# Kernel tuning notes

Hardware: AMD Instinct MI355X
Metric: run time of the kernel (lower is better)

The kernel has to match this reference:

```python
import jax, jax.numpy as jnp
import numpy as np

N = 100000   # nodes
E = 3200000  # edges (avg degree 32)
D = 128      # embed_dim
H = 512      # FF hidden
EPS = 1e-5   # BatchNorm eps


def setup_inputs() -> dict:
    key = jax.random.key(0)
    ks = jax.random.split(key, 10)
    x = jax.random.normal(ks[0], (N, D), dtype=jnp.float32)
    edge_index = jax.random.randint(ks[1], (2, E), 0, N, dtype=jnp.int32)
    s = 1.0 / np.sqrt(D)
    W = jax.random.uniform(ks[2], (D, D), jnp.float32, -s, s)   # GCNConv weight
    b = jnp.zeros((D,), jnp.float32)                             # GCNConv bias
    gamma = jnp.ones((D,), jnp.float32)                          # shared BN affine
    beta = jnp.zeros((D,), jnp.float32)
    s1 = 1.0 / np.sqrt(D)
    w1 = jax.random.uniform(ks[3], (D, H), jnp.float32, -s1, s1)
    b1 = jax.random.uniform(ks[4], (H,), jnp.float32, -s1, s1)
    s2 = 1.0 / np.sqrt(H)
    w2 = jax.random.uniform(ks[5], (H, D), jnp.float32, -s2, s2)
    b2 = jax.random.uniform(ks[6], (D,), jnp.float32, -s2, s2)
    return {"x": x, "edge_index": edge_index, "W": W, "b": b,
            "gamma": gamma, "beta": beta, "w1": w1, "b1": b1, "w2": w2, "b2": b2}


def batchnorm(x, gamma, beta):
    # training-mode BatchNorm1d over node dim, biased variance
    mu = jnp.mean(x, axis=0)
    var = jnp.mean(jnp.square(x - mu), axis=0)
    return (x - mu) * jax.lax.rsqrt(var + EPS) * gamma + beta


def gcn_conv(x, edge_index, W, b):
    # PyG GCNConv: add self-loops, sym-normalize, linear, scatter-add, bias
    n = x.shape[0]
    loops = jnp.arange(n, dtype=edge_index.dtype)
    src = jnp.concatenate([edge_index[0], loops])
    dst = jnp.concatenate([edge_index[1], loops])
    xw = x @ W                                                    # [N, D]
    deg = jax.ops.segment_sum(jnp.ones_like(dst, x.dtype), dst, num_segments=n)
    dinv = jax.lax.rsqrt(deg)                                     # deg >= 1 (self-loops)
    norm = dinv[src] * dinv[dst]                                  # [E+N]
    msg = xw[src] * norm[:, None]                                 # [E+N, D] gather
    out = jax.ops.segment_sum(msg, dst, num_segments=n)           # scatter-add
    return out + b


def reference(x, edge_index, W, b, gamma, beta, w1, b1, w2, b2):
    h = gcn_conv(x, edge_index, W, b)
    x = batchnorm(x + h, gamma, beta)
    ff = jax.nn.relu(x @ w1 + b1) @ w2 + b2
    return batchnorm(x + ff, gamma, beta)
```

## Files before the change

kernel.cpp:

```cpp
#include <hip/hip_runtime.h>
#include <hip/hip_bf16.h>
#include <stdint.h>

#define NN 100000
#define NE 3200000
#define DIM 128
#define HID 512
#define BN_EPS 1e-5f
#define NBIN 16
#define NPBIN 6250
#define TILE 2048
#define CAP 210000
#define GCNT 16

typedef short short8 __attribute__((ext_vector_type(8)));
typedef float floatx4 __attribute__((ext_vector_type(4)));

__device__ __forceinline__ float bfu2f(unsigned short u) {
    return __uint_as_float(((unsigned int)u) << 16);
}
__device__ __forceinline__ unsigned short f2bfu(float f) {
    union { __hip_bfloat16 h; unsigned short u; } cv;
    cv.h = __float2bfloat16(f);
    return cv.u;
}

__global__ void k_init(int* __restrict__ bincur, float* __restrict__ stats) {
    int i = blockIdx.x * 256 + threadIdx.x;
    if (i < NBIN) bincur[i] = i * CAP;
    if (i < 512) stats[i] = 0.f;
}

__global__ __launch_bounds__(256) void k_fill1(const int* __restrict__ src, const int* __restrict__ dst,
                                               int* __restrict__ bincur, unsigned int* __restrict__ recs) {
    __shared__ int lhist[NBIN], lbase[NBIN], gbase[NBIN];
    __shared__ unsigned int lrec[TILE];
    int tid = threadIdx.x;
    int tbase = blockIdx.x * TILE;
    if (tid < NBIN) lhist[tid] = 0;
    __syncthreads();
    unsigned int myrec[8];
    int mybin[8], myrank[8];
    #pragma unroll
    for (int j = 0; j < 8; ++j) {
        int e = tbase + j * 256 + tid;
        mybin[j] = -1;
        if (e < NE) {
            int d = __builtin_nontemporal_load(dst + e);
            int s = __builtin_nontemporal_load(src + e);
            int b = d / NPBIN;
            myrec[j] = (unsigned)s | ((unsigned)(d - b * NPBIN) << 17);
            mybin[j] = b;
            myrank[j] = atomicAdd(&lhist[b], 1);
        }
    }
    __syncthreads();
    if (tid == 0) {
        int run = 0;
        #pragma unroll
        for (int b = 0; b < NBIN; ++b) { lbase[b] = run; run += lhist[b]; }
    }
    __syncthreads();
    if (tid < NBIN) gbase[tid] = atomicAdd(&bincur[tid], lhist[tid]);
    __syncthreads();
    #pragma unroll
    for (int j = 0; j < 8; ++j)
        if (mybin[j] >= 0) lrec[lbase[mybin[j]] + myrank[j]] = myrec[j];
    __syncthreads();
    int total = lbase[NBIN - 1] + lhist[NBIN - 1];
    for (int i = tid; i < total; i += 256) {
        int b = 0;
        #pragma unroll
        for (int st = 8; st > 0; st >>= 1)
            if (b + st < NBIN && lbase[b + st] <= i) b += st;
        int p = gbase[b] + (i - lbase[b]);
        if (p < (b + 1) * CAP) recs[p] = lrec[i];
    }
}

__global__ __launch_bounds__(256) void k_cnt(const unsigned int* __restrict__ recs,
                                             const int* __restrict__ bincur,
                                             int* __restrict__ part) {
    __shared__ int lhist[NPBIN];
    int b = blockIdx.x & (NBIN - 1);
    int g = blockIdx.x >> 4;
    int tid = threadIdx.x;
    for (int i = tid; i < NPBIN; i += 256) lhist[i] = 0;
    __syncthreads();
    int start = b * CAP;
    int end = bincur[b];
    if (end > start + CAP) end = start + CAP;
    if (end < start) end = start;
    int n = end - start;
    int per = (n + GCNT - 1) / GCNT;
    int cbeg = start + g * per;
    int cend = min(cbeg + per, end);
    for (int i = cbeg + tid; i < cend; i += 256) {
        unsigned int r = __builtin_nontemporal_load(recs + i);
        int dl = (int)(r >> 17);
        if (dl < NPBIN) atomicAdd(&lhist[dl], 1);
    }
    __syncthreads();
    int* pp = part + (size_t)(b * GCNT + g) * NPBIN;
    for (int i = tid; i < NPBIN; i += 256) pp[i] = lhist[i];
}

__global__ void k_sum(const int* __restrict__ part, int* __restrict__ cnt) {
    int n = blockIdx.x * 256 + threadIdx.x;
    if (n < NN) {
        int b = n / NPBIN, dl = n - b * NPBIN;
        const int* pp = part + (size_t)b * GCNT * NPBIN + dl;
        int s = 0;
        #pragma unroll
        for (int g = 0; g < GCNT; ++g) s += pp[g * NPBIN];
        cnt[n] = s;
    }
}

__global__ __launch_bounds__(1024) void k_scanA(const int* __restrict__ cnt, int* __restrict__ offs,
                                                int* __restrict__ bsum, float* __restrict__ dinv) {
    __shared__ int wsum[16];
    int t = threadIdx.x;
    int lane = t & 63, wid = t >> 6;
    int i = blockIdx.x * 1024 + t;
    int v = (i < NN) ? cnt[i] : 0;
    int incl = v;
    #pragma unroll
    for (int off = 1; off < 64; off <<= 1) {
        int y = __shfl_up(incl, off, 64);
        if (lane >= off) incl += y;
    }
    if (lane == 63) wsum[wid] = incl;
    __syncthreads();
    if (wid == 0) {
        int wv = (lane < 16) ? wsum[lane] : 0;
        int wincl = wv;
        #pragma unroll
        for (int off = 1; off < 16; off <<= 1) {
            int y = __shfl_up(wincl, off, 64);
            if (lane >= off) wincl += y;
        }
        if (lane < 16) wsum[lane] = wincl - wv;
    }
    __syncthreads();
    int excl = wsum[wid] + incl - v;
    if (i < NN) {
        offs[i] = excl;
        dinv[i] = rsqrtf((float)(v + 1));
    }
    if (t == 1023) bsum[blockIdx.x] = excl + v;
}

__global__ __launch_bounds__(128) void k_scanB(int* __restrict__ bsum, int* __restrict__ offs, int nblk) {
    int t = threadIdx.x;
    if (t < 64) {
        int v = (t < nblk) ? bsum[t] : 0;
        int v2 = (t + 64 < nblk) ? bsum[t + 64] : 0;
        int incl = v;
        #pragma unroll
        for (int off = 1; off < 64; off <<= 1) {
            int y = __shfl_up(incl, off, 64);
            if (t >= off) incl += y;
        }
        int tot0 = __shfl(incl, 63, 64);
        int incl2 = v2;
        #pragma unroll
        for (int off = 1; off < 64; off <<= 1) {
            int y = __shfl_up(incl2, off, 64);
            if (t >= off) incl2 += y;
        }
        if (t < nblk) bsum[t] = incl - v;
        if (t + 64 < nblk) bsum[t + 64] = tot0 + incl2 - v2;
        if (t == 63) offs[NN] = tot0 + __shfl(incl2, 63, 64);
    }
}

__global__ void k_scanC(int* __restrict__ offs, const int* __restrict__ bsum, int* __restrict__ cur) {
    int i = blockIdx.x * 256 + threadIdx.x;
    if (i < NN) {
        int o = offs[i] + bsum[i >> 10];
        offs[i] = o;
        cur[i] = o;
    }
}

__global__ __launch_bounds__(256) void k_fill2(const unsigned int* __restrict__ recs,
                                               const int* __restrict__ bincur,
                                               int* __restrict__ cur, int* __restrict__ srcs) {
    int b = (blockIdx.x & 7) | (((blockIdx.x >> 3) & 1) << 3);
    int g = blockIdx.x >> 4;
    int lo = b * NPBIN;
    int start = b * CAP;
    int end = bincur[b];
    if (end > start + CAP) end = start + CAP;
    if (end < start) end = start;
    int nrec = end - start;
    int per = (nrec + 31) / 32;
    int cbeg = start + g * per;
    int cend = min(cbeg + per, end);
    for (int i = cbeg + threadIdx.x; i < cend; i += 256) {
        unsigned int r = __builtin_nontemporal_load(recs + i);
        int s = (int)(r & 0x1FFFFu);
        int d = lo + (int)(r >> 17);
        int p = atomicAdd(&cur[d], 1);
        if ((unsigned)p < NE) srcs[p] = s;
    }
}

__global__ void k_wt(const float* __restrict__ W, unsigned short* __restrict__ wt) {
    int i = blockIdx.x * 256 + threadIdx.x;
    if (i < DIM * DIM) {
        int k = i >> 7, n = i & 127;
        wt[n * DIM + k] = f2bfu(W[k * DIM + n]);
    }
}

__global__ void k_prep(const float* __restrict__ w1, const float* __restrict__ w2,
                       unsigned short* __restrict__ w1t, unsigned short* __restrict__ w2t) {
    int i = blockIdx.x * 256 + threadIdx.x;
    if (i < HID * DIM) {
        int n1 = i >> 7, k1 = i & 127;
        w1t[i] = f2bfu(w1[k1 * HID + n1]);
        int n2 = i & 127, k2 = i >> 7;
        w2t[n2 * HID + k2] = f2bfu(w2[k2 * DIM + n2]);
    }
}

__global__ __launch_bounds__(256) void k_gemm1(const float* __restrict__ x,
                                               const unsigned short* __restrict__ wt,
                                               const float* __restrict__ dinv,
                                               unsigned short* __restrict__ xw) {
    int wave = threadIdx.x >> 6;
    int lane = threadIdx.x & 63;
    int row0 = blockIdx.x * 64 + wave * 16;
    int arow = row0 + (lane & 15);
    if (arow >= NN) arow = NN - 1;
    int kbase = (lane >> 4) * 8;
    const float* xr = x + (size_t)arow * DIM;
    short8 afrag[4];
    #pragma unroll
    for (int kt = 0; kt < 4; ++kt) {
        float4 f0 = *(const float4*)(xr + kt * 32 + kbase);
        float4 f1 = *(const float4*)(xr + kt * 32 + kbase + 4);
        short8 a;
        a[0] = (short)f2bfu(f0.x); a[1] = (short)f2bfu(f0.y);
        a[2] = (short)f2bfu(f0.z); a[3] = (short)f2bfu(f0.w);
        a[4] = (short)f2bfu(f1.x); a[5] = (short)f2bfu(f1.y);
        a[6] = (short)f2bfu(f1.z); a[7] = (short)f2bfu(f1.w);
        afrag[kt] = a;
    }
    int crow = row0 + (lane >> 4) * 4;
    float dv[4];
    #pragma unroll
    for (int i = 0; i < 4; ++i) {
        int r = crow + i;
        dv[i] = dinv[r < NN ? r : NN - 1];
    }
    #pragma unroll
    for (int ct = 0; ct < 8; ++ct) {
        int ncol = ct * 16 + (lane & 15);
        const short* wr = (const short*)wt + (size_t)ncol * DIM;
        floatx4 acc = {0.f, 0.f, 0.f, 0.f};
        #pragma unroll
        for (int kt = 0; kt < 4; ++kt) {
            short8 bfrag = *(const short8*)(wr + kt * 32 + kbase);
            acc = __builtin_amdgcn_mfma_f32_16x16x32_bf16(afrag[kt], bfrag, acc, 0, 0, 0);
        }
        #pragma unroll
        for (int i = 0; i < 4; ++i) {
            int r = crow + i;
            if (r < NN) xw[(size_t)r * DIM + ct * 16 + (lane & 15)] = f2bfu(acc[i] * dv[i]);
        }
    }
}

__global__ __launch_bounds__(256) void k_aggregate(const unsigned int* __restrict__ xw2,
                                                   const int* __restrict__ offs,
                                                   const int* __restrict__ srcs,
                                                   const float* __restrict__ dinv,
                                                   const float* __restrict__ x,
                                                   const float* __restrict__ bias,
                                                   unsigned int* __restrict__ u) {
    int node = blockIdx.x * 4 + (threadIdx.x >> 6);
    if (node >= NN) return;
    int lane = threadIdx.x & 63;
    int qt = lane >> 4;
    int ql = lane & 15;
    int beg = offs[node], end = offs[node + 1];
    beg = max(0, min(beg, NE));
    end = max(beg, min(end, NE));
    int ne = end - beg;
    float a[8];
    #pragma unroll
    for (int j = 0; j < 8; ++j) a[j] = 0.f;
    const uint4* xw16 = (const uint4*)xw2;
    for (int base = 0; base < ne; base += 64) {
        int rem = ne - base;
        if (rem > 64) rem = 64;
        int sidx = (lane < rem) ? srcs[beg + base + lane] : 0;
        #pragma unroll 4
        for (int i = 0; i < rem; i += 4) {
            int want = i + qt;
            int s = __builtin_amdgcn_ds_bpermute(want << 2, sidx);
            if (want < rem) {
                if ((unsigned)s >= NN) s = 0;
                uint4 pk = xw16[(size_t)s * 16 + ql];
                a[0] += __uint_as_float(pk.x << 16);
                a[1] += __uint_as_float(pk.x & 0xffff0000u);
                a[2] += __uint_as_float(pk.y << 16);
                a[3] += __uint_as_float(pk.y & 0xffff0000u);
                a[4] += __uint_as_float(pk.z << 16);
                a[5] += __uint_as_float(pk.z & 0xffff0000u);
                a[6] += __uint_as_float(pk.w << 16);
                a[7] += __uint_as_float(pk.w & 0xffff0000u);
            }
        }
    }
    #pragma unroll
    for (int j = 0; j < 8; ++j) {
        a[j] += __shfl_xor(a[j], 16, 64);
        a[j] += __shfl_xor(a[j], 32, 64);
    }
    if (qt == 0) {
        uint4 ps = xw16[(size_t)node * 16 + ql];
        float di = dinv[node];
        const float* xr = x + (size_t)node * DIM + ql * 8;
        float4 xv0 = *(const float4*)xr;
        float4 xv1 = *(const float4*)(xr + 4);
        float4 bv0 = *(const float4*)(bias + ql * 8);
        float4 bv1 = *(const float4*)(bias + ql * 8 + 4);
        float o0 = xv0.x + bv0.x + di * (a[0] + __uint_as_float(ps.x << 16));
        float o1 = xv0.y + bv0.y + di * (a[1] + __uint_as_float(ps.x & 0xffff0000u));
        float o2 = xv0.z + bv0.z + di * (a[2] + __uint_as_float(ps.y << 16));
        float o3 = xv0.w + bv0.w + di * (a[3] + __uint_as_float(ps.y & 0xffff0000u));
        float o4 = xv1.x + bv1.x + di * (a[4] + __uint_as_float(ps.z << 16));
        float o5 = xv1.y + bv1.y + di * (a[5] + __uint_as_float(ps.z & 0xffff0000u));
        float o6 = xv1.z + bv1.z + di * (a[6] + __uint_as_float(ps.w << 16));
        float o7 = xv1.w + bv1.w + di * (a[7] + __uint_as_float(ps.w & 0xffff0000u));
        uint4 pk;
        pk.x = ((unsigned int)f2bfu(o1) << 16) | (unsigned int)f2bfu(o0);
        pk.y = ((unsigned int)f2bfu(o3) << 16) | (unsigned int)f2bfu(o2);
        pk.z = ((unsigned int)f2bfu(o5) << 16) | (unsigned int)f2bfu(o4);
        pk.w = ((unsigned int)f2bfu(o7) << 16) | (unsigned int)f2bfu(o6);
        ((uint4*)u)[(size_t)node * 16 + ql] = pk;
    }
}

__global__ void k_stats(const unsigned int* __restrict__ u2, float* __restrict__ stats) {
    int t = threadIdx.x;
    int c = t & 63, g = t >> 6;
    float s0 = 0.f, q0 = 0.f, s1 = 0.f, q1 = 0.f;
    for (int r = blockIdx.x * 4 + g; r < NN; r += gridDim.x * 4) {
        unsigned int pv = u2[(size_t)r * 64 + c];
        float x0 = __uint_as_float(pv << 16);
        float x1 = __uint_as_float(pv & 0xffff0000u);
        s0 += x0; q0 += x0 * x0; s1 += x1; q1 += x1 * x1;
    }
    __shared__ float A[256], B[256], C[256], D2[256];
    A[t] = s0; B[t] = q0; C[t] = s1; D2[t] = q1;
    __syncthreads();
    if (t < 64) {
        float rs0 = A[t] + A[t + 64] + A[t + 128] + A[t + 192];
        float rq0 = B[t] + B[t + 64] + B[t + 128] + B[t + 192];
        float rs1 = C[t] + C[t + 64] + C[t + 128] + C[t + 192];
        float rq1 = D2[t] + D2[t + 64] + D2[t + 128] + D2[t + 192];
        atomicAdd(&stats[2 * c],           rs0);
        atomicAdd(&stats[2 * c + 1],       rs1);
        atomicAdd(&stats[DIM + 2 * c],     rq0);
        atomicAdd(&stats[DIM + 2 * c + 1], rq1);
    }
}

__global__ void k_stats2(const float2* __restrict__ v2, float* __restrict__ stats) {
    int t = threadIdx.x;
    int c = t & 63, g = t >> 6;
    float s0 = 0.f, q0 = 0.f, s1 = 0.f, q1 = 0.f;
    for (int r = blockIdx.x * 4 + g; r < NN; r += gridDim.x * 4) {
        float2 pv = v2[(size_t)r * 64 + c];
        s0 += pv.x; q0 += pv.x * pv.x; s1 += pv.y; q1 += pv.y * pv.y;
    }
    __shared__ float A[256], B[256], C[256], D2[256];
    A[t] = s0; B[t] = q0; C[t] = s1; D2[t] = q1;
    __syncthreads();
    if (t < 64) {
        float rs0 = A[t] + A[t + 64] + A[t + 128] + A[t + 192];
        float rq0 = B[t] + B[t + 64] + B[t + 128] + B[t + 192];
        float rs1 = C[t] + C[t + 64] + C[t + 128] + C[t + 192];
        float rq1 = D2[t] + D2[t + 64] + D2[t + 128] + D2[t + 192];
        atomicAdd(&stats[2 * c],           rs0);
        atomicAdd(&stats[2 * c + 1],       rs1);
        atomicAdd(&stats[DIM + 2 * c],     rq0);
        atomicAdd(&stats[DIM + 2 * c + 1], rq1);
    }
}

__global__ __launch_bounds__(256) void k_ffx(const unsigned int* __restrict__ u2,
                                             const float* __restrict__ stats1,
                                             const float* __restrict__ gamma,
                                             const float* __restrict__ beta,
                                             const unsigned short* __restrict__ w1t,
                                             const float* __restrict__ b1,
                                             const unsigned short* __restrict__ w2t,
                                             const float* __restrict__ b2,
                                             float* __restrict__ v) {
    __shared__ __align__(16) float sscale[DIM], sshift[DIM];
    __shared__ __align__(16) unsigned int sw1[64 * 64];
    __shared__ __align__(16) unsigned int sw2[128 * 32];
    __shared__ __align__(16) unsigned int hbufs[4][16 * 32];
    int tid = threadIdx.x;
    if (tid < DIM) {
        float mu  = stats1[tid] * (1.0f / NN);
        float var = stats1[DIM + tid] * (1.0f / NN) - mu * mu;
        float sc = rsqrtf(var + BN_EPS) * gamma[tid];
        sscale[tid] = sc;
        sshift[tid] = beta[tid] - mu * sc;
    }
    __syncthreads();
    int wave = tid >> 6, lane = tid & 63;
    int m = lane & 15, q = lane >> 4;
    int nb = blockIdx.x * 128 + wave * 32;
    unsigned int* hb = &hbufs[wave][0];
    const int xsw = (m & 7) * 4;

    short8 yfrag[2][4];
    #pragma unroll
    for (int s = 0; s < 2; ++s) {
        int ng = nb + s * 16 + m;
        if (ng >= NN) ng = NN - 1;
        const uint4* up = (const uint4*)(u2 + (size_t)ng * 64);
        #pragma unroll
        for (int kt = 0; kt < 4; ++kt) {
            uint4 pv = up[kt * 4 + q];
            int c0 = kt * 32 + q * 8;
            float4 sa = *(const float4*)&sscale[c0], sb = *(const float4*)&sscale[c0 + 4];
            float4 ha = *(const float4*)&sshift[c0], hbv = *(const float4*)&sshift[c0 + 4];
            float f0 = __uint_as_float(pv.x << 16)         * sa.x + ha.x;
            float f1 = __uint_as_float(pv.x & 0xffff0000u) * sa.y + ha.y;
            float f2 = __uint_as_float(pv.y << 16)         * sa.z + ha.z;
            float f3 = __uint_as_float(pv.y & 0xffff0000u) * sa.w + ha.w;
            float f4 = __uint_as_float(pv.z << 16)         * sb.x + hbv.x;
            float f5 = __uint_as_float(pv.z & 0xffff0000u) * sb.y + hbv.y;
            float f6 = __uint_as_float(pv.w << 16)         * sb.z + hbv.z;
            float f7 = __uint_as_float(pv.w & 0xffff0000u) * sb.w + hbv.w;
            union { unsigned int u[4]; short8 sv; } yf;
            yf.u[0] = ((unsigned int)f2bfu(f1) << 16) | f2bfu(f0);
            yf.u[1] = ((unsigned int)f2bfu(f3) << 16) | f2bfu(f2);
            yf.u[2] = ((unsigned int)f2bfu(f5) << 16) | f2bfu(f4);
            yf.u[3] = ((unsigned int)f2bfu(f7) << 16) | f2bfu(f6);
            yfrag[s][kt] = yf.sv;
        }
    }

    floatx4 acc2[2][8];
    #pragma unroll
    for (int s = 0; s < 2; ++s)
        #pragma unroll
        for (int t = 0; t < 8; ++t) acc2[s][t] = (floatx4){0.f, 0.f, 0.f, 0.f};

    const uint4* w1g = (const uint4*)w1t;
    const uint4* w2g = (const uint4*)w2t;

    for (int c = 0; c < 8; ++c) {
        __syncthreads();
        #pragma unroll
        for (int it = 0; it < 4; ++it) {
            int i = tid + it * 256;
            int j = i >> 4, s4 = i & 15;
            uint4 val = w1g[(size_t)(c * 64 + j) * 16 + s4];
            *(uint4*)&sw1[j * 64 + ((s4 * 4) ^ ((j & 7) * 4))] = val;
        }
        #pragma unroll
        for (int it = 0; it < 4; ++it) {
            int i = tid + it * 256;
            int n = i >> 3, s4 = i & 7;
            uint4 val = w2g[(size_t)n * 64 + c * 8 + s4];
            *(uint4*)&sw2[n * 32 + ((s4 * 4) ^ ((n & 7) * 4))] = val;
        }
        __syncthreads();
        #pragma unroll
        for (int s = 0; s < 2; ++s) {
            floatx4 acc1[4];
            #pragma unroll
            for (int t = 0; t < 4; ++t) acc1[t] = (floatx4){0.f, 0.f, 0.f, 0.f};
            #pragma unroll
            for (int kt = 0; kt < 4; ++kt) {
                #pragma unroll
                for (int t = 0; t < 4; ++t) {
                    short8 wf = *(const short8*)&sw1[(t * 16 + m) * 64 + ((kt * 16 + q * 4) ^ xsw)];
                    acc1[t] = __builtin_amdgcn_mfma_f32_16x16x32_bf16(wf, yfrag[s][kt], acc1[t], 0, 0, 0);
                }
            }
            #pragma unroll
            for (int t = 0; t < 4; ++t) {
                float4 bb = *(const float4*)&b1[c * 64 + t * 16 + q * 4];
                float h0 = fmaxf(acc1[t][0] + bb.x, 0.f);
                float h1 = fmaxf(acc1[t][1] + bb.y, 0.f);
                float h2 = fmaxf(acc1[t][2] + bb.z, 0.f);
                float h3 = fmaxf(acc1[t][3] + bb.w, 0.f);
                uint2 hp;
                hp.x = ((unsigned int)f2bfu(h1) << 16) | f2bfu(h0);
                hp.y = ((unsigned int)f2bfu(h3) << 16) | f2bfu(h2);
                *(uint2*)&hb[m * 32 + ((t * 8 + q * 2) ^ xsw)] = hp;
            }
            #pragma unroll
            for (int kt = 0; kt < 2; ++kt) {
                short8 hf = *(const short8*)&hb[m * 32 + ((kt * 16 + q * 4) ^ xsw)];
                #pragma unroll
                for (int t = 0; t < 8; ++t) {
                    short8 wf2 = *(const short8*)&sw2[(t * 16 + m) * 32 + ((kt * 16 + q * 4) ^ xsw)];
                    acc2[s][t] = __builtin_amdgcn_mfma_f32_16x16x32_bf16(hf, wf2, acc2[s][t], 0, 0, 0);
                }
            }
        }
    }
    #pragma unroll
    for (int s = 0; s < 2; ++s) {
        #pragma unroll
        for (int t = 0; t < 8; ++t) {
            int col = t * 16 + m;
            float b2v = b2[col];
            float scl = sscale[col], shf = sshift[col];
            #pragma unroll
            for (int i = 0; i < 4; ++i) {
                int ng = nb + s * 16 + q * 4 + i;
                if (ng < NN) {
                    unsigned int pv = u2[(size_t)ng * 64 + (col >> 1)];
                    float uval = (col & 1) ? __uint_as_float(pv & 0xffff0000u)
                                           : __uint_as_float(pv << 16);
                    v[(size_t)ng * DIM + col] = acc2[s][t][i] + b2v + (uval * scl + shf);
                }
            }
        }
    }
}

__global__ void k_final(float* buf, const float* __restrict__ stats2,
                        const float* __restrict__ gamma,
                        const float* __restrict__ beta) {
    __shared__ float ssc[DIM], ssh[DIM];
    int t = threadIdx.x;
    if (t < DIM) {
        float mu  = stats2[t] * (1.0f / NN);
        float var = stats2[DIM + t] * (1.0f / NN) - mu * mu;
        float rsg = rsqrtf(var + BN_EPS) * gamma[t];
        ssc[t] = rsg;
        ssh[t] = beta[t] - mu * rsg;
    }
    __syncthreads();
    const int total = NN * DIM / 4;
    float4* b4 = (float4*)buf;
    for (int i = blockIdx.x * blockDim.x + t; i < total; i += gridDim.x * blockDim.x) {
        float4 val = b4[i];
        int c = (i * 4) & (DIM - 1);
        val.x = val.x * ssc[c]     + ssh[c];
        val.y = val.y * ssc[c + 1] + ssh[c + 1];
        val.z = val.z * ssc[c + 2] + ssh[c + 2];
        val.w = val.w * ssc[c + 3] + ssh[c + 3];
        b4[i] = val;
    }
}

extern "C" void kernel_launch(void* const* d_in, const int* in_sizes, int n_in,
                              void* d_out, int out_size, void* d_ws, size_t ws_size,
                              hipStream_t stream) {
    const float* x     = (const float*)d_in[0];
    const int*   ei    = (const int*)d_in[1];
    const float* W     = (const float*)d_in[2];
    const float* b     = (const float*)d_in[3];
    const float* gamma = (const float*)d_in[4];
    const float* beta  = (const float*)d_in[5];
    const float* w1    = (const float*)d_in[6];
    const float* b1    = (const float*)d_in[7];
    const float* w2    = (const float*)d_in[8];
    const float* b2    = (const float*)d_in[9];

    char* p = (char*)d_ws;
    auto alloc = [&](size_t bytes) { char* r = p; p += (bytes + 255) & ~(size_t)255; return r; };
    unsigned int*   u     = (unsigned int*)alloc((size_t)NN * DIM * 2);
    int*            cnt   = (int*)alloc((size_t)NN * 4);
    int*            offs  = (int*)alloc((size_t)(NN + 1) * 4);
    int*            cur   = (int*)alloc((size_t)NN * 4);
    float*          dinv  = (float*)alloc((size_t)NN * 4);
    int*            bsum  = (int*)alloc(128 * 4);
    int*            bincur = (int*)alloc((size_t)NBIN * 4);
    unsigned short* wt    = (unsigned short*)alloc((size_t)DIM * DIM * 2);
    unsigned short* w1t   = (unsigned short*)alloc((size_t)HID * DIM * 2);
    unsigned short* w2t   = (unsigned short*)alloc((size_t)HID * DIM * 2);
    float*          stats = (float*)alloc(512 * 4);

    unsigned short* xw   = (unsigned short*)d_out;
    unsigned int*   recs = (unsigned int*)d_out;
    int*            srcs = (int*)((char*)d_out + (size_t)NN * DIM * 2);
    int*            part = (int*)((char*)d_out + (size_t)NN * DIM * 2 + (size_t)NE * 4);
    float*          v    = (float*)d_out;

    const int* esrc = ei;
    const int* edst = ei + NE;
    const int nblk = (NN + 1023) / 1024;
    const int n1blk = (NE + TILE - 1) / TILE;

    k_init<<<2, 256, 0, stream>>>(bincur, stats);
    k_fill1<<<n1blk, 256, 0, stream>>>(esrc, edst, bincur, recs);
    k_cnt<<<NBIN * GCNT, 256, 0, stream>>>(recs, bincur, part);
    k_sum<<<(NN + 255) / 256, 256, 0, stream>>>(part, cnt);
    k_scanA<<<nblk, 1024, 0, stream>>>(cnt, offs, bsum, dinv);
    k_scanB<<<1, 128, 0, stream>>>(bsum, offs, nblk);
    k_scanC<<<(NN + 255) / 256, 256, 0, stream>>>(offs, bsum, cur);
    k_fill2<<<512, 256, 0, stream>>>(recs, bincur, cur, srcs);
    k_wt<<<(DIM * DIM + 255) / 256, 256, 0, stream>>>(W, wt);
    k_prep<<<(HID * DIM + 255) / 256, 256, 0, stream>>>(w1, w2, w1t, w2t);
    k_gemm1<<<(NN + 63) / 64, 256, 0, stream>>>(x, wt, dinv, xw);
    k_aggregate<<<(NN + 3) / 4, 256, 0, stream>>>((const unsigned int*)xw, offs, srcs, dinv, x, b, u);
    k_stats<<<512, 256, 0, stream>>>(u, stats);
    k_ffx<<<(NN + 127) / 128, 256, 0, stream>>>(u, stats, gamma, beta, w1t, b1, w2t, b2, v);
    k_stats2<<<512, 256, 0, stream>>>((const float2*)v, stats + 256);
    k_final<<<2048, 256, 0, stream>>>((float*)d_out, stats + 256, gamma, beta);
}
```

Before: 663.1 us.

## Use finer destination bins so counting and CSR fill run in LDS

Raises the destination bin count from 16 to 128 so each bin's node range fits in shared memory. Per-bin histogram blocks then write counts directly, which drops the partial-count buffer and the k_sum reduction kernel. The CSR fill uses LDS cursors seeded from the scanned offsets instead of global atomics on a cur array, and k_scanC no longer writes cur. In exchange only 128 blocks run in k_cnt and k_fill2, with one block per bin, so parallelism drops and per-block serial work grows. The smaller per-bin capacity (CAP 27000 against an average of about 25000 records per bin) raises the risk of silently dropping edges from skewed bins.

```diff
diff --git a/kernel.cpp b/kernel.cpp
--- a/kernel.cpp
+++ b/kernel.cpp
@@ -7,11 +7,10 @@
 #define DIM 128
 #define HID 512
 #define BN_EPS 1e-5f
-#define NBIN 16
-#define NPBIN 6250
+#define NBIN 128
+#define NPBIN 784
 #define TILE 2048
-#define CAP 210000
-#define GCNT 16
+#define CAP 27000
 
 typedef short short8 __attribute__((ext_vector_type(8)));
 typedef float floatx4 __attribute__((ext_vector_type(4)));
@@ -71,7 +70,7 @@
     for (int i = tid; i < total; i += 256) {
         int b = 0;
         #pragma unroll
-        for (int st = 8; st > 0; st >>= 1)
+        for (int st = NBIN / 2; st > 0; st >>= 1)
             if (b + st < NBIN && lbase[b + st] <= i) b += st;
         int p = gbase[b] + (i - lbase[b]);
         if (p < (b + 1) * CAP) recs[p] = lrec[i];
@@ -80,10 +79,9 @@
 
 __global__ __launch_bounds__(256) void k_cnt(const unsigned int* __restrict__ recs,
                                              const int* __restrict__ bincur,
-                                             int* __restrict__ part) {
+                                             int* __restrict__ cnt) {
     __shared__ int lhist[NPBIN];
-    int b = blockIdx.x & (NBIN - 1);
-    int g = blockIdx.x >> 4;
+    int b = blockIdx.x;
     int tid = threadIdx.x;
     for (int i = tid; i < NPBIN; i += 256) lhist[i] = 0;
     __syncthreads();
@@ -91,29 +89,15 @@
     int end = bincur[b];
     if (end > start + CAP) end = start + CAP;
     if (end < start) end = start;
-    int n = end - start;
-    int per = (n + GCNT - 1) / GCNT;
-    int cbeg = start + g * per;
-    int cend = min(cbeg + per, end);
-    for (int i = cbeg + tid; i < cend; i += 256) {
+    for (int i = start + tid; i < end; i += 256) {
         unsigned int r = __builtin_nontemporal_load(recs + i);
         int dl = (int)(r >> 17);
         if (dl < NPBIN) atomicAdd(&lhist[dl], 1);
     }
     __syncthreads();
-    int* pp = part + (size_t)(b * GCNT + g) * NPBIN;
-    for (int i = tid; i < NPBIN; i += 256) pp[i] = lhist[i];
-}
-
-__global__ void k_sum(const int* __restrict__ part, int* __restrict__ cnt) {
-    int n = blockIdx.x * 256 + threadIdx.x;
-    if (n < NN) {
-        int b = n / NPBIN, dl = n - b * NPBIN;
-        const int* pp = part + (size_t)b * GCNT * NPBIN + dl;
-        int s = 0;
-        #pragma unroll
-        for (int g = 0; g < GCNT; ++g) s += pp[g * NPBIN];
-        cnt[n] = s;
+    for (int i = tid; i < NPBIN; i += 256) {
+        int n = b * NPBIN + i;
+        if (n < NN) cnt[n] = lhist[i];
     }
 }
 
@@ -175,35 +159,36 @@
     }
 }
 
-__global__ void k_scanC(int* __restrict__ offs, const int* __restrict__ bsum, int* __restrict__ cur) {
+__global__ void k_scanC(int* __restrict__ offs, const int* __restrict__ bsum) {
     int i = blockIdx.x * 256 + threadIdx.x;
-    if (i < NN) {
-        int o = offs[i] + bsum[i >> 10];
-        offs[i] = o;
-        cur[i] = o;
-    }
+    if (i < NN) offs[i] += bsum[i >> 10];
 }
 
 __global__ __launch_bounds__(256) void k_fill2(const unsigned int* __restrict__ recs,
                                                const int* __restrict__ bincur,
-                                               int* __restrict__ cur, int* __restrict__ srcs) {
-    int b = (blockIdx.x & 7) | (((blockIdx.x >> 3) & 1) << 3);
-    int g = blockIdx.x >> 4;
-    int lo = b * NPBIN;
+                                               const int* __restrict__ offs,
+                                               int* __restrict__ srcs) {
+    __shared__ int loffs[NPBIN], lcur[NPBIN];
+    int b = blockIdx.x;
+    int tid = threadIdx.x;
+    for (int i = tid; i < NPBIN; i += 256) {
+        int n = b * NPBIN + i;
+        loffs[i] = (n <= NN) ? offs[n] : NE;
+        lcur[i] = 0;
+    }
+    __syncthreads();
     int start = b * CAP;
     int end = bincur[b];
     if (end > start + CAP) end = start + CAP;
     if (end < start) end = start;
-    int nrec = end - start;
-    int per = (nrec + 31) / 32;
-    int cbeg = start + g * per;
-    int cend = min(cbeg + per, end);
-    for (int i = cbeg + threadIdx.x; i < cend; i += 256) {
+    for (int i = start + tid; i < end; i += 256) {
         unsigned int r = __builtin_nontemporal_load(recs + i);
         int s = (int)(r & 0x1FFFFu);
-        int d = lo + (int)(r >> 17);
-        int p = atomicAdd(&cur[d], 1);
-        if ((unsigned)p < NE) srcs[p] = s;
+        int dl = (int)(r >> 17);
+        if (dl < NPBIN) {
+            int p = loffs[dl] + atomicAdd(&lcur[dl], 1);
+            if ((unsigned)p < NE) srcs[p] = s;
+        }
     }
 }
 
@@ -579,7 +564,6 @@
     unsigned int*   u     = (unsigned int*)alloc((size_t)NN * DIM * 2);
     int*            cnt   = (int*)alloc((size_t)NN * 4);
     int*            offs  = (int*)alloc((size_t)(NN + 1) * 4);
-    int*            cur   = (int*)alloc((size_t)NN * 4);
     float*          dinv  = (float*)alloc((size_t)NN * 4);
     int*            bsum  = (int*)alloc(128 * 4);
     int*            bincur = (int*)alloc((size_t)NBIN * 4);
@@ -591,7 +575,6 @@
     unsigned short* xw   = (unsigned short*)d_out;
     unsigned int*   recs = (unsigned int*)d_out;
     int*            srcs = (int*)((char*)d_out + (size_t)NN * DIM * 2);
-    int*            part = (int*)((char*)d_out + (size_t)NN * DIM * 2 + (size_t)NE * 4);
     float*          v    = (float*)d_out;
 
     const int* esrc = ei;
@@ -601,12 +584,11 @@
 
     k_init<<<2, 256, 0, stream>>>(bincur, stats);
     k_fill1<<<n1blk, 256, 0, stream>>>(esrc, edst, bincur, recs);
-    k_cnt<<<NBIN * GCNT, 256, 0, stream>>>(recs, bincur, part);
-    k_sum<<<(NN + 255) / 256, 256, 0, stream>>>(part, cnt);
+    k_cnt<<<NBIN, 256, 0, stream>>>(recs, bincur, cnt);
     k_scanA<<<nblk, 1024, 0, stream>>>(cnt, offs, bsum, dinv);
     k_scanB<<<1, 128, 0, stream>>>(bsum, offs, nblk);
-    k_scanC<<<(NN + 255) / 256, 256, 0, stream>>>(offs, bsum, cur);
-    k_fill2<<<512, 256, 0, stream>>>(recs, bincur, cur, srcs);
+    k_scanC<<<(NN + 255) / 256, 256, 0, stream>>>(offs, bsum);
+    k_fill2<<<NBIN, 256, 0, stream>>>(recs, bincur, offs, srcs);
     k_wt<<<(DIM * DIM + 255) / 256, 256, 0, stream>>>(W, wt);
     k_prep<<<(HID * DIM + 255) / 256, 256, 0, stream>>>(w1, w2, w1t, w2t);
     k_gemm1<<<(NN + 63) / 64, 256, 0, stream>>>(x, wt, dinv, xw);
```

After: 596.0 us. 10.1% less time.
